# Kernel optimization log

Hardware: AMD Instinct MI355X
Metric: run time of the kernel (lower is better)

The kernel has to match this reference:

```python
import jax, jax.numpy as jnp
import numpy as np

D_MODEL = 1024
NUM_HEADS = 16
D_K = D_MODEL // NUM_HEADS
THETA = 10000.0
BATCH = 2
SEQ = 2048


def apply_rope(x, token_positions):
    # x: [B, H, S, D_K]; token_positions: [S] int
    half = D_K // 2
    inv_freq = THETA ** (-(jnp.arange(half, dtype=jnp.float32) * 2.0) / D_K)  # [half]
    angles = token_positions.astype(jnp.float32)[:, None] * inv_freq[None, :]  # [S, half]
    cos = jnp.cos(angles)  # [S, half]
    sin = jnp.sin(angles)
    x1 = x[..., 0::2]  # even indices
    x2 = x[..., 1::2]  # odd indices
    out_even = x1 * cos - x2 * sin
    out_odd = x1 * sin + x2 * cos
    # interleave back: [..., S, half, 2] -> [..., S, D_K]
    return jnp.stack([out_even, out_odd], axis=-1).reshape(x.shape)


def setup_inputs() -> dict:
    key = jax.random.key(0)
    ks = jax.random.split(key, 5)
    x = jax.random.normal(ks[0], (BATCH, SEQ, D_MODEL), dtype=jnp.float32)
    token_positions = jnp.arange(SEQ, dtype=jnp.int64)
    scale = 0.02
    Wq = jax.random.normal(ks[1], (D_MODEL, D_MODEL), dtype=jnp.float32) * scale
    Wk = jax.random.normal(ks[2], (D_MODEL, D_MODEL), dtype=jnp.float32) * scale
    Wv = jax.random.normal(ks[3], (D_MODEL, D_MODEL), dtype=jnp.float32) * scale
    Wo = jax.random.normal(ks[4], (D_MODEL, D_MODEL), dtype=jnp.float32) * scale
    return {"x": x, "token_positions": token_positions, "Wq": Wq, "Wk": Wk, "Wv": Wv, "Wo": Wo}


def reference(x, token_positions, Wq, Wk, Wv, Wo):
    B, S, _ = x.shape
    # cs336 Linear: y = x @ W.T with W of shape (out, in), no bias
    def proj(W):
        h = jnp.einsum('bsd,od->bso', x, W)
        return h.reshape(B, S, NUM_HEADS, D_K).transpose(0, 2, 1, 3)  # [B,H,S,Dk]
    Q = apply_rope(proj(Wq), token_positions)
    K = apply_rope(proj(Wk), token_positions)
    V = proj(Wv)
    scores = jnp.einsum('bhqd,bhkd->bhqk', Q, K) / jnp.sqrt(jnp.float32(D_K))
    causal = jnp.tril(jnp.ones((S, S), dtype=bool))
    scores = jnp.where(causal, scores, -jnp.inf)
    attn = jax.nn.softmax(scores, axis=-1)
    out = jnp.einsum('bhqk,bhkd->bhqd', attn, V)  # [B,H,S,Dk]
    out = out.transpose(0, 2, 1, 3).reshape(B, S, D_MODEL)
    return jnp.einsum('bsd,od->bso', out, Wo)
```

## Files before the change

kernel.cpp:

```cpp
#include <hip/hip_runtime.h>
#include <hip/hip_bf16.h>
#include <math.h>

#define NHEADS 16
#define DKH 64
#define SEQ 2048
#define DMODEL 1024

typedef __attribute__((ext_vector_type(8))) short short8;
typedef __attribute__((ext_vector_type(4))) float f32x4;

#define GLDS16(g, l)                                         \
  __builtin_amdgcn_global_load_lds(                          \
      (__attribute__((address_space(1))) void*)(void*)(g),   \
      (__attribute__((address_space(3))) void*)(l), 16, 0, 0)

__device__ __forceinline__ short f2bf(float f) {
  unsigned u = __float_as_uint(f);
  unsigned r = (u + 0x7fffu + ((u >> 16) & 1u)) >> 16;
  return (short)r;
}

__device__ __forceinline__ short8 pack8(float4 a, float4 b) {
  short8 v;
  v[0] = f2bf(a.x); v[1] = f2bf(a.y); v[2] = f2bf(a.z); v[3] = f2bf(a.w);
  v[4] = f2bf(b.x); v[5] = f2bf(b.y); v[6] = f2bf(b.z); v[7] = f2bf(b.w);
  return v;
}

__device__ __forceinline__ int swz(int r, int gran) {
  return r * 64 + ((gran ^ (r & 7)) << 3);
}

__global__ void rope_table_kernel(const int* __restrict__ tp,
                                  float* __restrict__ ct, float* __restrict__ st) {
  int idx = blockIdx.x * 256 + threadIdx.x;
  if (idx >= SEQ * 32) return;
  int s = idx >> 5, i = idx & 31;
  int is64 = (tp[1] == 0);
  int p = is64 ? tp[2 * s] : tp[s];
  float invf = powf(10000.0f, -(2.0f * (float)i) / 64.0f);
  float a = (float)p * invf;
  ct[idx] = cosf(a);
  st[idx] = sinf(a);
}

__global__ __launch_bounds__(256) void precast_kernel(
    const float* __restrict__ X, const float* __restrict__ Wq,
    const float* __restrict__ Wk, const float* __restrict__ Wv,
    const float* __restrict__ Wo,
    short* __restrict__ Xb, short* __restrict__ Wqb, short* __restrict__ Wkb,
    short* __restrict__ Wvb, short* __restrict__ Wob) {
  int i = blockIdx.x * 256 + threadIdx.x;
  const float* src; short* dst; int off;
  if (i < 524288) { src = X; dst = Xb; off = i; }
  else {
    int k = i - 524288; int w = k >> 17; off = k & 131071;
    src = (w == 0) ? Wq : (w == 1) ? Wk : (w == 2) ? Wv : Wo;
    dst = (w == 0) ? Wqb : (w == 1) ? Wkb : (w == 2) ? Wvb : Wob;
  }
  const float4* p = reinterpret_cast<const float4*>(src) + 2 * (size_t)off;
  float4 a = p[0], b = p[1];
  reinterpret_cast<short8*>(dst)[off] = pack8(a, b);
}

__global__ __launch_bounds__(256) void gemm_qkv_kernel(
    const short* __restrict__ X, const short* __restrict__ Wq,
    const short* __restrict__ Wk, const short* __restrict__ Wv,
    short* __restrict__ Qb, short* __restrict__ Kb, short* __restrict__ Vb,
    const float* __restrict__ ct, const float* __restrict__ st) {
  __shared__ __align__(16) short As[128 * 64];
  __shared__ __align__(16) short Bs[128 * 64];
  const int tm = blockIdx.x;
  const int tn = blockIdx.y;
  const int tid = threadIdx.x;
  const int wave = tid >> 6, lane = tid & 63;
  const int l15 = lane & 15, quad = lane >> 4;
  const int wm = wave >> 1, wn = wave & 1;

  const int mid = tn >> 3;
  const int n0 = (tn & 7) * 128;
  const short* W = (mid == 0) ? Wq : (mid == 1 ? Wk : Wv);
  const short* Abase = X + (size_t)(tm * 128) * DMODEL;
  const short* Bbase = W + (size_t)n0 * DMODEL;

  const int lr = lane >> 3;
  const int lc = (lane & 7) ^ lr;

  f32x4 acc[4][4];
#pragma unroll
  for (int mb = 0; mb < 4; mb++)
#pragma unroll
    for (int nb = 0; nb < 4; nb++) acc[mb][nb] = (f32x4){0.f, 0.f, 0.f, 0.f};

  for (int kk = 0; kk < 16; kk++) {
    const short* Ak = Abase + kk * 64;
    const short* Bk = Bbase + kk * 64;
#pragma unroll
    for (int i = 0; i < 4; i++) {
      int R = i * 32 + wave * 8;
      GLDS16(Ak + (size_t)(R + lr) * DMODEL + lc * 8, &As[R * 64 + lane * 8]);
    }
#pragma unroll
    for (int i = 0; i < 4; i++) {
      int R = i * 32 + wave * 8;
      GLDS16(Bk + (size_t)(R + lr) * DMODEL + lc * 8, &Bs[R * 64 + lane * 8]);
    }
    __syncthreads();
#pragma unroll
    for (int kg = 0; kg < 2; kg++) {
      short8 af[4], bf[4];
#pragma unroll
      for (int mb = 0; mb < 4; mb++) {
        int r = wm * 64 + mb * 16 + l15;
        af[mb] = *reinterpret_cast<const short8*>(&As[swz(r, kg * 4 + quad)]);
      }
#pragma unroll
      for (int nb = 0; nb < 4; nb++) {
        int r = wn * 64 + nb * 16 + l15;
        bf[nb] = *reinterpret_cast<const short8*>(&Bs[swz(r, kg * 4 + quad)]);
      }
#pragma unroll
      for (int mb = 0; mb < 4; mb++)
#pragma unroll
        for (int nb = 0; nb < 4; nb++)
          acc[mb][nb] = __builtin_amdgcn_mfma_f32_16x16x32_bf16(af[mb], bf[nb], acc[mb][nb], 0, 0, 0);
    }
    __syncthreads();
  }

#pragma unroll
  for (int mb = 0; mb < 4; mb++)
#pragma unroll
    for (int nb = 0; nb < 4; nb++) {
      int nl = n0 + wn * 64 + nb * 16 + l15;
      int h = nl >> 6, dd = nl & 63;
#pragma unroll
      for (int reg = 0; reg < 4; reg++) {
        int rg = tm * 128 + wm * 64 + mb * 16 + quad * 4 + reg;
        int b = rg >> 11, s = rg & 2047;
        float v = acc[mb][nb][reg];
        size_t oi = (((size_t)(b * NHEADS + h)) * SEQ + s) * DKH + dd;
        if (mid == 2) {
          Vb[oi] = f2bf(v);
        } else {
          float pv = __shfl_xor(v, 1);
          int fi = dd >> 1;
          float c = ct[s * 32 + fi], sn = st[s * 32 + fi];
          float o = (dd & 1) ? (pv * sn + v * c) : (v * c - pv * sn);
          ((mid == 0) ? Qb : Kb)[oi] = f2bf(o);
        }
      }
    }
}

__global__ __launch_bounds__(256, 4) void attn_kernel(
    const short* __restrict__ Qb, const short* __restrict__ Kb,
    const short* __restrict__ Vb, short* __restrict__ Ob) {
  __shared__ __align__(16) short QPs[64 * 64];
  __shared__ __align__(16) short Ks[2][64 * 64];
  __shared__ __align__(16) short Vs[2][64 * 64];

  const int id = blockIdx.x;
  const int xx = id & 7;
  const int mm = (((id >> 3) & 3) + (id >> 8)) & 3;
  const int bh = id >> 5;
  const int qt = (mm == 0) ? (31 - xx) : (mm == 1) ? (16 + xx)
               : (mm == 2) ? (15 - xx) : xx;

  const int tid = threadIdx.x;
  const int wave = tid >> 6, lane = tid & 63;
  const int l15 = lane & 15, quad = lane >> 4;
  const int sr0 = tid >> 3, sc = tid & 7;

  const short* Qp = Qb + (size_t)bh * SEQ * DKH;
  const short* Kp = Kb + (size_t)bh * SEQ * DKH;
  const short* Vp = Vb + (size_t)bh * SEQ * DKH;

  uint4 kreg[2], vreg[2];
#pragma unroll
  for (int i = 0; i < 2; i++) {
    int r = sr0 + i * 32;
    kreg[i] = *reinterpret_cast<const uint4*>(Kp + (size_t)r * DKH + sc * 8);
    vreg[i] = *reinterpret_cast<const uint4*>(Vp + (size_t)r * DKH + sc * 8);
  }
#pragma unroll
  for (int i = 0; i < 2; i++) {
    int r = sr0 + i * 32;
    uint4 v = *reinterpret_cast<const uint4*>(Qp + (size_t)(qt * 64 + r) * DKH + sc * 8);
    *reinterpret_cast<uint4*>(&QPs[swz(r, sc)]) = v;
  }
#pragma unroll
  for (int i = 0; i < 2; i++) {
    int r = sr0 + i * 32;
    *reinterpret_cast<uint4*>(&Ks[0][swz(r, sc)]) = kreg[i];
    const short* vsp = reinterpret_cast<const short*>(&vreg[i]);
#pragma unroll
    for (int j = 0; j < 8; j++) {
      int dv = sc * 8 + j;
      Vs[0][dv * 64 + ((((r >> 3) ^ (dv & 7) ^ (dv >> 3)) & 7) << 3) + (r & 7)] = vsp[j];
    }
  }
  __syncthreads();
  short8 qf0, qf1;
  {
    int r = wave * 16 + l15;
    qf0 = *reinterpret_cast<const short8*>(&QPs[swz(r, quad)]);
    qf1 = *reinterpret_cast<const short8*>(&QPs[swz(r, 4 + quad)]);
  }

  f32x4 accO[4];
#pragma unroll
  for (int i = 0; i < 4; i++) accO[i] = (f32x4){0.f, 0.f, 0.f, 0.f};
  float rs[4] = {0.f, 0.f, 0.f, 0.f};

  const float SCL = 0.125f * 1.44269504089f;
  const float FM = 13.0f;

  int buf = 0;
  for (int kt = 0; kt <= qt; kt++) {
    if (kt < qt) {
#pragma unroll
      for (int i = 0; i < 2; i++) {
        int r = (kt + 1) * 64 + sr0 + i * 32;
        kreg[i] = *reinterpret_cast<const uint4*>(Kp + (size_t)r * DKH + sc * 8);
        vreg[i] = *reinterpret_cast<const uint4*>(Vp + (size_t)r * DKH + sc * 8);
      }
    }

    f32x4 sa[4];
#pragma unroll
    for (int nb = 0; nb < 4; nb++) {
      sa[nb] = (f32x4){0.f, 0.f, 0.f, 0.f};
      int r = nb * 16 + l15;
      short8 kf0 = *reinterpret_cast<const short8*>(&Ks[buf][swz(r, quad)]);
      sa[nb] = __builtin_amdgcn_mfma_f32_16x16x32_bf16(qf0, kf0, sa[nb], 0, 0, 0);
      short8 kf1 = *reinterpret_cast<const short8*>(&Ks[buf][swz(r, 4 + quad)]);
      sa[nb] = __builtin_amdgcn_mfma_f32_16x16x32_bf16(qf1, kf1, sa[nb], 0, 0, 0);
    }

    const bool diag = (kt == qt);
#pragma unroll
    for (int nb = 0; nb < 4; nb++)
#pragma unroll
      for (int reg = 0; reg < 4; reg++) {
        float p = exp2f(sa[nb][reg] * SCL - FM);
        if (diag && (nb * 16 + l15) > (wave * 16 + quad * 4 + reg)) p = 0.f;
        rs[reg] += p;
        int r = quad * 4 + reg, col = nb * 16 + l15;
        QPs[swz(wave * 16 + r, col >> 3) + (col & 7)] = f2bf(p);
      }

    short8 pf0, pf1;
    {
      int r = wave * 16 + l15;
      pf0 = *reinterpret_cast<const short8*>(&QPs[swz(r, quad)]);
      pf1 = *reinterpret_cast<const short8*>(&QPs[swz(r, 4 + quad)]);
    }
#pragma unroll
    for (int db = 0; db < 4; db++) {
      int dv = db * 16 + l15;
      int fsw = (dv & 7) ^ (dv >> 3);
      short8 vf0 = *reinterpret_cast<const short8*>(
          &Vs[buf][dv * 64 + (((quad ^ fsw) & 7) << 3)]);
      accO[db] = __builtin_amdgcn_mfma_f32_16x16x32_bf16(pf0, vf0, accO[db], 0, 0, 0);
      short8 vf1 = *reinterpret_cast<const short8*>(
          &Vs[buf][dv * 64 + ((((quad + 4) ^ fsw) & 7) << 3)]);
      accO[db] = __builtin_amdgcn_mfma_f32_16x16x32_bf16(pf1, vf1, accO[db], 0, 0, 0);
    }

    if (kt < qt) {
      int nbuf = buf ^ 1;
#pragma unroll
      for (int i = 0; i < 2; i++) {
        int r = sr0 + i * 32;
        *reinterpret_cast<uint4*>(&Ks[nbuf][swz(r, sc)]) = kreg[i];
        const short* vsp = reinterpret_cast<const short*>(&vreg[i]);
#pragma unroll
        for (int j = 0; j < 8; j++) {
          int dv = sc * 8 + j;
          Vs[nbuf][dv * 64 + ((((r >> 3) ^ (dv & 7) ^ (dv >> 3)) & 7) << 3) + (r & 7)] = vsp[j];
        }
      }
      __syncthreads();
      buf = nbuf;
    }
  }

  float lrow[4];
#pragma unroll
  for (int reg = 0; reg < 4; reg++) {
    float t = rs[reg];
#pragma unroll
    for (int off = 1; off < 16; off <<= 1) t += __shfl_xor(t, off);
    lrow[reg] = t;
  }

  int b = bh >> 4, h = bh & 15;
#pragma unroll
  for (int db = 0; db < 4; db++)
#pragma unroll
    for (int reg = 0; reg < 4; reg++) {
      int s = qt * 64 + wave * 16 + quad * 4 + reg;
      int dv = db * 16 + l15;
      float o = accO[db][reg] / lrow[reg];
      Ob[((size_t)(b * SEQ + s)) * DMODEL + h * DKH + dv] = f2bf(o);
    }
}

__global__ __launch_bounds__(256) void gemm_out_kernel(
    const short* __restrict__ X, const short* __restrict__ Wo, float* __restrict__ Out) {
  __shared__ __align__(16) short As[128 * 64];
  __shared__ __align__(16) short Bs[64 * 64];
  const int tm = blockIdx.x;
  const int tn = blockIdx.y;
  const int tid = threadIdx.x;
  const int wave = tid >> 6, lane = tid & 63;
  const int l15 = lane & 15, quad = lane >> 4;
  const int wm = wave >> 1, wn = wave & 1;

  const short* Abase = X + (size_t)(tm * 128) * DMODEL;
  const short* Bbase = Wo + (size_t)(tn * 64) * DMODEL;

  const int lr = lane >> 3;
  const int lc = (lane & 7) ^ lr;

  f32x4 acc[4][2];
#pragma unroll
  for (int mb = 0; mb < 4; mb++)
#pragma unroll
    for (int nb = 0; nb < 2; nb++) acc[mb][nb] = (f32x4){0.f, 0.f, 0.f, 0.f};

  for (int kk = 0; kk < 16; kk++) {
    const short* Ak = Abase + kk * 64;
    const short* Bk = Bbase + kk * 64;
#pragma unroll
    for (int i = 0; i < 4; i++) {
      int R = i * 32 + wave * 8;
      GLDS16(Ak + (size_t)(R + lr) * DMODEL + lc * 8, &As[R * 64 + lane * 8]);
    }
#pragma unroll
    for (int i = 0; i < 2; i++) {
      int R = i * 32 + wave * 8;
      GLDS16(Bk + (size_t)(R + lr) * DMODEL + lc * 8, &Bs[R * 64 + lane * 8]);
    }
    __syncthreads();
#pragma unroll
    for (int kg = 0; kg < 2; kg++) {
      short8 af[4], bf[2];
#pragma unroll
      for (int mb = 0; mb < 4; mb++) {
        int r = wm * 64 + mb * 16 + l15;
        af[mb] = *reinterpret_cast<const short8*>(&As[swz(r, kg * 4 + quad)]);
      }
#pragma unroll
      for (int nb = 0; nb < 2; nb++) {
        int r = wn * 32 + nb * 16 + l15;
        bf[nb] = *reinterpret_cast<const short8*>(&Bs[swz(r, kg * 4 + quad)]);
      }
#pragma unroll
      for (int mb = 0; mb < 4; mb++)
#pragma unroll
        for (int nb = 0; nb < 2; nb++)
          acc[mb][nb] = __builtin_amdgcn_mfma_f32_16x16x32_bf16(af[mb], bf[nb], acc[mb][nb], 0, 0, 0);
    }
    __syncthreads();
  }
#pragma unroll
  for (int mb = 0; mb < 4; mb++)
#pragma unroll
    for (int nb = 0; nb < 2; nb++)
#pragma unroll
      for (int reg = 0; reg < 4; reg++) {
        int rg = tm * 128 + wm * 64 + mb * 16 + quad * 4 + reg;
        int col = tn * 64 + wn * 32 + nb * 16 + l15;
        Out[(size_t)rg * DMODEL + col] = acc[mb][nb][reg];
      }
}

extern "C" void kernel_launch(void* const* d_in, const int* in_sizes, int n_in,
                              void* d_out, int out_size, void* d_ws, size_t ws_size,
                              hipStream_t stream) {
  (void)in_sizes; (void)n_in; (void)out_size; (void)ws_size;
  const float* X  = (const float*)d_in[0];
  const int*   tp = (const int*)d_in[1];
  const float* Wq = (const float*)d_in[2];
  const float* Wk = (const float*)d_in[3];
  const float* Wv = (const float*)d_in[4];
  const float* Wo = (const float*)d_in[5];
  float* Out = (float*)d_out;

  short* Qb  = (short*)d_ws;
  short* Kb  = Qb + 4194304;
  short* Vb  = Kb + 4194304;
  short* Ab  = Vb + 4194304;
  short* Xb  = Ab + 4194304;
  short* Wqb = Xb + 4194304;
  short* Wkb = Wqb + 1048576;
  short* Wvb = Wkb + 1048576;
  short* Wob = Wvb + 1048576;
  float* ct  = (float*)(Wob + 1048576);
  float* st  = ct + SEQ * 32;

  rope_table_kernel<<<dim3(256), dim3(256), 0, stream>>>(tp, ct, st);
  precast_kernel<<<dim3(4096), dim3(256), 0, stream>>>(X, Wq, Wk, Wv, Wo,
                                                       Xb, Wqb, Wkb, Wvb, Wob);
  gemm_qkv_kernel<<<dim3(32, 24), dim3(256), 0, stream>>>(Xb, Wqb, Wkb, Wvb,
                                                          Qb, Kb, Vb, ct, st);
  attn_kernel<<<dim3(1024), dim3(256), 0, stream>>>(Qb, Kb, Vb, Ab);
  gemm_out_kernel<<<dim3(32, 16), dim3(256), 0, stream>>>(Ab, Wob, Out);
}
```

Baseline: 217.9 us.

## Store V transposed from QKV GEMM, compute S^T in attention, fuse rope into precast

The QKV GEMM epilogue now writes V in a transposed [bh, d, seq] layout using packed 8-byte stores. This lets the attention kernel load V tiles with plain vector LDS stores instead of scattered per-element transposing writes. The attention score MFMA swaps its operands to produce S^T, so each lane holds four consecutive keys for one query row. P is then written to LDS as packed uint2, and the row sum becomes a single accumulator reduced with two shuffles plus a broadcast. The rope table kernel is merged into the precast kernel, saving one launch. The cost is that Q/K rope stores in the epilogue remain scalar.

```diff
diff --git a/kernel.cpp b/kernel.cpp
--- a/kernel.cpp
+++ b/kernel.cpp
@@ -32,36 +32,37 @@
   return r * 64 + ((gran ^ (r & 7)) << 3);
 }
 
-__global__ void rope_table_kernel(const int* __restrict__ tp,
-                                  float* __restrict__ ct, float* __restrict__ st) {
-  int idx = blockIdx.x * 256 + threadIdx.x;
-  if (idx >= SEQ * 32) return;
-  int s = idx >> 5, i = idx & 31;
-  int is64 = (tp[1] == 0);
-  int p = is64 ? tp[2 * s] : tp[s];
-  float invf = powf(10000.0f, -(2.0f * (float)i) / 64.0f);
-  float a = (float)p * invf;
-  ct[idx] = cosf(a);
-  st[idx] = sinf(a);
-}
-
-__global__ __launch_bounds__(256) void precast_kernel(
+__global__ __launch_bounds__(256) void precast_rope_kernel(
     const float* __restrict__ X, const float* __restrict__ Wq,
     const float* __restrict__ Wk, const float* __restrict__ Wv,
-    const float* __restrict__ Wo,
+    const float* __restrict__ Wo, const int* __restrict__ tp,
     short* __restrict__ Xb, short* __restrict__ Wqb, short* __restrict__ Wkb,
-    short* __restrict__ Wvb, short* __restrict__ Wob) {
-  int i = blockIdx.x * 256 + threadIdx.x;
-  const float* src; short* dst; int off;
-  if (i < 524288) { src = X; dst = Xb; off = i; }
-  else {
-    int k = i - 524288; int w = k >> 17; off = k & 131071;
-    src = (w == 0) ? Wq : (w == 1) ? Wk : (w == 2) ? Wv : Wo;
-    dst = (w == 0) ? Wqb : (w == 1) ? Wkb : (w == 2) ? Wvb : Wob;
-  }
-  const float4* p = reinterpret_cast<const float4*>(src) + 2 * (size_t)off;
-  float4 a = p[0], b = p[1];
-  reinterpret_cast<short8*>(dst)[off] = pack8(a, b);
+    short* __restrict__ Wvb, short* __restrict__ Wob,
+    float* __restrict__ ct, float* __restrict__ st) {
+  int bid = blockIdx.x;
+  if (bid < 4096) {
+    int i = bid * 256 + threadIdx.x;
+    const float* src; short* dst; int off;
+    if (i < 524288) { src = X; dst = Xb; off = i; }
+    else {
+      int k = i - 524288; int w = k >> 17; off = k & 131071;
+      src = (w == 0) ? Wq : (w == 1) ? Wk : (w == 2) ? Wv : Wo;
+      dst = (w == 0) ? Wqb : (w == 1) ? Wkb : (w == 2) ? Wvb : Wob;
+    }
+    const float4* p = reinterpret_cast<const float4*>(src) + 2 * (size_t)off;
+    float4 a = p[0], b = p[1];
+    reinterpret_cast<short8*>(dst)[off] = pack8(a, b);
+  } else {
+    int idx = (bid - 4096) * 256 + threadIdx.x;
+    if (idx >= SEQ * 32) return;
+    int s = idx >> 5, i = idx & 31;
+    int is64 = (tp[1] == 0);
+    int p = is64 ? tp[2 * s] : tp[s];
+    float invf = powf(10000.0f, -(2.0f * (float)i) / 64.0f);
+    float a = (float)p * invf;
+    ct[idx] = cosf(a);
+    st[idx] = sinf(a);
+  }
 }
 
 __global__ __launch_bounds__(256) void gemm_qkv_kernel(
@@ -130,33 +131,40 @@
   }
 
 #pragma unroll
-  for (int mb = 0; mb < 4; mb++)
+  for (int mb = 0; mb < 4; mb++) {
+    const int s0g = tm * 128 + wm * 64 + mb * 16 + quad * 4;
+    const int b = s0g >> 11, s = s0g & 2047;
 #pragma unroll
     for (int nb = 0; nb < 4; nb++) {
       int nl = n0 + wn * 64 + nb * 16 + l15;
       int h = nl >> 6, dd = nl & 63;
-#pragma unroll
-      for (int reg = 0; reg < 4; reg++) {
-        int rg = tm * 128 + wm * 64 + mb * 16 + quad * 4 + reg;
-        int b = rg >> 11, s = rg & 2047;
-        float v = acc[mb][nb][reg];
-        size_t oi = (((size_t)(b * NHEADS + h)) * SEQ + s) * DKH + dd;
-        if (mid == 2) {
-          Vb[oi] = f2bf(v);
-        } else {
+      if (mid == 2) {
+        unsigned u0 = (unsigned)(unsigned short)f2bf(acc[mb][nb][0]) |
+                      ((unsigned)(unsigned short)f2bf(acc[mb][nb][1]) << 16);
+        unsigned u1 = (unsigned)(unsigned short)f2bf(acc[mb][nb][2]) |
+                      ((unsigned)(unsigned short)f2bf(acc[mb][nb][3]) << 16);
+        uint2 pk; pk.x = u0; pk.y = u1;
+        *reinterpret_cast<uint2*>(Vb + ((size_t)(b * NHEADS + h) * DKH + dd) * SEQ + s) = pk;
+      } else {
+#pragma unroll
+        for (int reg = 0; reg < 4; reg++) {
+          float v = acc[mb][nb][reg];
           float pv = __shfl_xor(v, 1);
           int fi = dd >> 1;
-          float c = ct[s * 32 + fi], sn = st[s * 32 + fi];
+          int sg = s + reg;
+          float c = ct[sg * 32 + fi], sn = st[sg * 32 + fi];
           float o = (dd & 1) ? (pv * sn + v * c) : (v * c - pv * sn);
+          size_t oi = (((size_t)(b * NHEADS + h)) * SEQ + sg) * DKH + dd;
           ((mid == 0) ? Qb : Kb)[oi] = f2bf(o);
         }
       }
     }
+  }
 }
 
 __global__ __launch_bounds__(256, 4) void attn_kernel(
     const short* __restrict__ Qb, const short* __restrict__ Kb,
-    const short* __restrict__ Vb, short* __restrict__ Ob) {
+    const short* __restrict__ Vtb, short* __restrict__ Ob) {
   __shared__ __align__(16) short QPs[64 * 64];
   __shared__ __align__(16) short Ks[2][64 * 64];
   __shared__ __align__(16) short Vs[2][64 * 64];
@@ -175,14 +183,14 @@
 
   const short* Qp = Qb + (size_t)bh * SEQ * DKH;
   const short* Kp = Kb + (size_t)bh * SEQ * DKH;
-  const short* Vp = Vb + (size_t)bh * SEQ * DKH;
+  const short* Vp = Vtb + (size_t)bh * DKH * SEQ;
 
   uint4 kreg[2], vreg[2];
 #pragma unroll
   for (int i = 0; i < 2; i++) {
     int r = sr0 + i * 32;
     kreg[i] = *reinterpret_cast<const uint4*>(Kp + (size_t)r * DKH + sc * 8);
-    vreg[i] = *reinterpret_cast<const uint4*>(Vp + (size_t)r * DKH + sc * 8);
+    vreg[i] = *reinterpret_cast<const uint4*>(Vp + (size_t)r * SEQ + sc * 8);
   }
 #pragma unroll
   for (int i = 0; i < 2; i++) {
@@ -194,12 +202,7 @@
   for (int i = 0; i < 2; i++) {
     int r = sr0 + i * 32;
     *reinterpret_cast<uint4*>(&Ks[0][swz(r, sc)]) = kreg[i];
-    const short* vsp = reinterpret_cast<const short*>(&vreg[i]);
-#pragma unroll
-    for (int j = 0; j < 8; j++) {
-      int dv = sc * 8 + j;
-      Vs[0][dv * 64 + ((((r >> 3) ^ (dv & 7) ^ (dv >> 3)) & 7) << 3) + (r & 7)] = vsp[j];
-    }
+    *reinterpret_cast<uint4*>(&Vs[0][swz(r, sc)]) = vreg[i];
   }
   __syncthreads();
   short8 qf0, qf1;
@@ -212,7 +215,7 @@
   f32x4 accO[4];
 #pragma unroll
   for (int i = 0; i < 4; i++) accO[i] = (f32x4){0.f, 0.f, 0.f, 0.f};
-  float rs[4] = {0.f, 0.f, 0.f, 0.f};
+  float rs = 0.f;
 
   const float SCL = 0.125f * 1.44269504089f;
   const float FM = 13.0f;
@@ -222,9 +225,9 @@
     if (kt < qt) {
 #pragma unroll
       for (int i = 0; i < 2; i++) {
-        int r = (kt + 1) * 64 + sr0 + i * 32;
-        kreg[i] = *reinterpret_cast<const uint4*>(Kp + (size_t)r * DKH + sc * 8);
-        vreg[i] = *reinterpret_cast<const uint4*>(Vp + (size_t)r * DKH + sc * 8);
+        int r = sr0 + i * 32;
+        kreg[i] = *reinterpret_cast<const uint4*>(Kp + (size_t)((kt + 1) * 64 + r) * DKH + sc * 8);
+        vreg[i] = *reinterpret_cast<const uint4*>(Vp + (size_t)r * SEQ + (kt + 1) * 64 + sc * 8);
       }
     }
 
@@ -234,38 +237,44 @@
       sa[nb] = (f32x4){0.f, 0.f, 0.f, 0.f};
       int r = nb * 16 + l15;
       short8 kf0 = *reinterpret_cast<const short8*>(&Ks[buf][swz(r, quad)]);
-      sa[nb] = __builtin_amdgcn_mfma_f32_16x16x32_bf16(qf0, kf0, sa[nb], 0, 0, 0);
+      sa[nb] = __builtin_amdgcn_mfma_f32_16x16x32_bf16(kf0, qf0, sa[nb], 0, 0, 0);
       short8 kf1 = *reinterpret_cast<const short8*>(&Ks[buf][swz(r, 4 + quad)]);
-      sa[nb] = __builtin_amdgcn_mfma_f32_16x16x32_bf16(qf1, kf1, sa[nb], 0, 0, 0);
+      sa[nb] = __builtin_amdgcn_mfma_f32_16x16x32_bf16(kf1, qf1, sa[nb], 0, 0, 0);
     }
 
     const bool diag = (kt == qt);
-#pragma unroll
-    for (int nb = 0; nb < 4; nb++)
-#pragma unroll
-      for (int reg = 0; reg < 4; reg++) {
-        float p = exp2f(sa[nb][reg] * SCL - FM);
-        if (diag && (nb * 16 + l15) > (wave * 16 + quad * 4 + reg)) p = 0.f;
-        rs[reg] += p;
-        int r = quad * 4 + reg, col = nb * 16 + l15;
-        QPs[swz(wave * 16 + r, col >> 3) + (col & 7)] = f2bf(p);
-      }
-
-    short8 pf0, pf1;
-    {
-      int r = wave * 16 + l15;
-      pf0 = *reinterpret_cast<const short8*>(&QPs[swz(r, quad)]);
-      pf1 = *reinterpret_cast<const short8*>(&QPs[swz(r, 4 + quad)]);
-    }
+    const int prow = wave * 16 + l15;
+#pragma unroll
+    for (int nb = 0; nb < 4; nb++) {
+      float p0 = exp2f(sa[nb][0] * SCL - FM);
+      float p1 = exp2f(sa[nb][1] * SCL - FM);
+      float p2 = exp2f(sa[nb][2] * SCL - FM);
+      float p3 = exp2f(sa[nb][3] * SCL - FM);
+      if (diag) {
+        int kbase = nb * 16 + quad * 4;
+        if (kbase + 0 > prow) p0 = 0.f;
+        if (kbase + 1 > prow) p1 = 0.f;
+        if (kbase + 2 > prow) p2 = 0.f;
+        if (kbase + 3 > prow) p3 = 0.f;
+      }
+      rs += (p0 + p1) + (p2 + p3);
+      unsigned u0 = (unsigned)(unsigned short)f2bf(p0) |
+                    ((unsigned)(unsigned short)f2bf(p1) << 16);
+      unsigned u1 = (unsigned)(unsigned short)f2bf(p2) |
+                    ((unsigned)(unsigned short)f2bf(p3) << 16);
+      uint2 pk; pk.x = u0; pk.y = u1;
+      int g = 2 * nb + (quad >> 1);
+      *reinterpret_cast<uint2*>(&QPs[swz(prow, g) + (quad & 1) * 4]) = pk;
+    }
+
+    short8 pf0 = *reinterpret_cast<const short8*>(&QPs[swz(prow, quad)]);
+    short8 pf1 = *reinterpret_cast<const short8*>(&QPs[swz(prow, 4 + quad)]);
 #pragma unroll
     for (int db = 0; db < 4; db++) {
       int dv = db * 16 + l15;
-      int fsw = (dv & 7) ^ (dv >> 3);
-      short8 vf0 = *reinterpret_cast<const short8*>(
-          &Vs[buf][dv * 64 + (((quad ^ fsw) & 7) << 3)]);
+      short8 vf0 = *reinterpret_cast<const short8*>(&Vs[buf][swz(dv, quad)]);
       accO[db] = __builtin_amdgcn_mfma_f32_16x16x32_bf16(pf0, vf0, accO[db], 0, 0, 0);
-      short8 vf1 = *reinterpret_cast<const short8*>(
-          &Vs[buf][dv * 64 + ((((quad + 4) ^ fsw) & 7) << 3)]);
+      short8 vf1 = *reinterpret_cast<const short8*>(&Vs[buf][swz(dv, 4 + quad)]);
       accO[db] = __builtin_amdgcn_mfma_f32_16x16x32_bf16(pf1, vf1, accO[db], 0, 0, 0);
     }
 
@@ -275,26 +284,19 @@
       for (int i = 0; i < 2; i++) {
         int r = sr0 + i * 32;
         *reinterpret_cast<uint4*>(&Ks[nbuf][swz(r, sc)]) = kreg[i];
-        const short* vsp = reinterpret_cast<const short*>(&vreg[i]);
-#pragma unroll
-        for (int j = 0; j < 8; j++) {
-          int dv = sc * 8 + j;
-          Vs[nbuf][dv * 64 + ((((r >> 3) ^ (dv & 7) ^ (dv >> 3)) & 7) << 3) + (r & 7)] = vsp[j];
-        }
+        *reinterpret_cast<uint4*>(&Vs[nbuf][swz(r, sc)]) = vreg[i];
       }
       __syncthreads();
       buf = nbuf;
     }
   }
 
-  float lrow[4];
-#pragma unroll
-  for (int reg = 0; reg < 4; reg++) {
-    float t = rs[reg];
-#pragma unroll
-    for (int off = 1; off < 16; off <<= 1) t += __shfl_xor(t, off);
-    lrow[reg] = t;
-  }
+  float t = rs;
+  t += __shfl_xor(t, 16);
+  t += __shfl_xor(t, 32);
+  float lv[4];
+#pragma unroll
+  for (int reg = 0; reg < 4; reg++) lv[reg] = __shfl(t, quad * 4 + reg);
 
   int b = bh >> 4, h = bh & 15;
 #pragma unroll
@@ -303,7 +305,7 @@
     for (int reg = 0; reg < 4; reg++) {
       int s = qt * 64 + wave * 16 + quad * 4 + reg;
       int dv = db * 16 + l15;
-      float o = accO[db][reg] / lrow[reg];
+      float o = accO[db][reg] / lv[reg];
       Ob[((size_t)(b * SEQ + s)) * DMODEL + h * DKH + dv] = f2bf(o);
     }
 }
@@ -402,9 +404,8 @@
   float* ct  = (float*)(Wob + 1048576);
   float* st  = ct + SEQ * 32;
 
-  rope_table_kernel<<<dim3(256), dim3(256), 0, stream>>>(tp, ct, st);
-  precast_kernel<<<dim3(4096), dim3(256), 0, stream>>>(X, Wq, Wk, Wv, Wo,
-                                                       Xb, Wqb, Wkb, Wvb, Wob);
+  precast_rope_kernel<<<dim3(4352), dim3(256), 0, stream>>>(
+      X, Wq, Wk, Wv, Wo, tp, Xb, Wqb, Wkb, Wvb, Wob, ct, st);
   gemm_qkv_kernel<<<dim3(32, 24), dim3(256), 0, stream>>>(Xb, Wqb, Wkb, Wvb,
                                                           Qb, Kb, Vb, ct, st);
   attn_kernel<<<dim3(1024), dim3(256), 0, stream>>>(Qb, Kb, Vb, Ab);
```

Result: faster. 187.9 us (-13.8%).
